# Kernel optimization log

Hardware: AMD Instinct MI355X
Metric: run time of the kernel (lower is better)

Reference implementation:

```python
import jax, jax.numpy as jnp
import numpy as np

B, S, H = 2, 4096, 1024
NH, BS, NR = 16, 64, 3
HD = H // NH
NB = S // BS
PEN = -10000.0


def setup_inputs():
    key = jax.random.key(0)
    k0, k1, k2, k3 = jax.random.split(key, 4)
    s = 0.02
    inp = {
        'hidden_states': jax.random.normal(k0, (B, S, H), jnp.float32),
        'attention_mask': jnp.ones((B, S), jnp.float32),
        'Wq': jax.random.normal(k1, (H, H), jnp.float32) * s,
        'Wk': jax.random.normal(k2, (H, H), jnp.float32) * s,
        'Wv': jax.random.normal(k3, (H, H), jnp.float32) * s,
        'bq': jnp.zeros((H,), jnp.float32),
        'bk': jnp.zeros((H,), jnp.float32),
        'bv': jnp.zeros((H,), jnp.float32),
    }
    rng = np.random.default_rng(0)
    inp['rand_attn'] = jnp.asarray(rng.integers(1, NB - 1, size=(B, NH, NB - 2, NR)), jnp.int32)
    return inp


def _attend(q_blk, kmat, vmat, mask, rsd):
    # q_blk:[b,h,q,d]  kmat/vmat:[b,h,k,d]  mask: multiplicative {0,1} broadcastable to [b,h,q,k]
    p = jnp.einsum('bhqd,bhkd->bhqk', q_blk, kmat) * rsd + (1.0 - mask) * PEN
    return jnp.einsum('bhqk,bhkd->bhqd', jax.nn.softmax(p, axis=-1), vmat)


def reference(hidden_states, attention_mask, Wq, bq, Wk, bk, Wv, bv, rand_attn):
    b, s, _ = hidden_states.shape
    h, d, bs = NH, HD, BS
    nb = s // bs
    rsd = 1.0 / jnp.sqrt(jnp.asarray(d, hidden_states.dtype))

    def proj(W, bias):
        return (hidden_states @ W + bias).reshape(b, s, h, d).transpose(0, 2, 1, 3)

    q, k, v = proj(Wq, bq), proj(Wk, bk), proj(Wv, bv)  # [b,h,s,d]

    # --- masks (create_masks_for_block_sparse_attn)
    bm = attention_mask.reshape(b, nb, bs)
    band_mask = jnp.einsum('blq,blk->blqk', bm[:, 2:-2],
                           jnp.concatenate([bm[:, 1:-3], bm[:, 2:-2], bm[:, 3:-1]], axis=2))[:, None]
    from_mask = attention_mask.reshape(b, 1, s, 1)
    to_mask = attention_mask.reshape(b, 1, 1, s)

    qb = q.reshape(b, h, nb, bs, d)
    kb = k.reshape(b, h, nb, bs, d)
    vb = v.reshape(b, h, nb, bs, d)

    # --- gather random blocks (jax_gather with batch_dims=2)
    gather2 = jax.vmap(jax.vmap(lambda m, i: m[i]))
    gk = gather2(kb, rand_attn).reshape(b, h, nb - 2, NR * bs, d)
    gv = gather2(vb, rand_attn).reshape(b, h, nb - 2, NR * bs, d)
    rm = jax.vmap(lambda m, i: m[i])(bm, rand_attn).reshape(b, h, nb - 2, NR * bs)
    rand_mask = jnp.einsum('blq,bhlk->bhlqk', bm[:, 1:-1], rm)  # [b,h,nb-2,bs,NR*bs]

    # --- block 0: attends to everything
    first_ctx = _attend(qb[:, :, 0], k, v, to_mask, rsd)[:, :, None]

    # --- block 1: first 3 blocks + last block + its random blocks
    ones_r = jnp.ones((b, 1, 1, NR * bs), q.dtype)
    sk = jnp.concatenate([kb[:, :, 0], kb[:, :, 1], kb[:, :, 2], kb[:, :, -1], gk[:, :, 0]], axis=2)
    sv = jnp.concatenate([vb[:, :, 0], vb[:, :, 1], vb[:, :, 2], vb[:, :, -1], gv[:, :, 0]], axis=2)
    seq_pad = jnp.concatenate([to_mask[:, :, :, :3 * bs], to_mask[:, :, :, -bs:], ones_r], axis=3)
    rand_pad = jnp.concatenate([jnp.ones((b, h, bs, 4 * bs), q.dtype), rand_mask[:, :, 0]], axis=3)
    second_ctx = _attend(qb[:, :, 1], sk, sv, jnp.minimum(seq_pad, rand_pad), rsd)[:, :, None]

    # --- middle blocks 2..nb-3: sliding band + random + first-global + last-global
    mq = qb[:, :, 2:-2]  # [b,h,L,bs,d], L = nb-4
    ek = jnp.concatenate([kb[:, :, 1:-3], kb[:, :, 2:-2], kb[:, :, 3:-1]], axis=3)  # [b,h,L,3bs,d]
    ev = jnp.concatenate([vb[:, :, 1:-3], vb[:, :, 2:-2], vb[:, :, 3:-1]], axis=3)
    band_p = jnp.einsum('bhlqd,bhlkd->bhlqk', mq, ek) * rsd + (1.0 - band_mask) * PEN
    rand_p = jnp.einsum('bhlqd,bhlkd->bhlqk', mq, gk[:, :, 1:-1]) * rsd + (1.0 - rand_mask[:, :, 1:-1]) * PEN
    first_p = jnp.einsum('bhlqd,bhkd->bhlqk', mq, kb[:, :, 0]) * rsd \
        + (1.0 - to_mask[:, :, :, :bs][:, :, :, None]) * PEN
    last_p = jnp.einsum('bhlqd,bhkd->bhlqk', mq, kb[:, :, -1]) * rsd \
        + (1.0 - to_mask[:, :, :, -bs:][:, :, :, None]) * PEN
    # scores layout: [first(bs) | band(3bs) | rand(NR*bs) | last(bs)]
    w = jax.nn.softmax(jnp.concatenate([first_p, band_p, rand_p, last_p], axis=-1), axis=-1)
    mid_ctx = jnp.einsum('bhlqk,bhlkd->bhlqd', w[..., bs:4 * bs], ev)
    mid_ctx += jnp.einsum('bhlqk,bhlkd->bhlqd', w[..., 4 * bs:-bs], gv[:, :, 1:-1])
    mid_ctx += jnp.einsum('bhlqk,bhkd->bhlqd', w[..., :bs], vb[:, :, 0])
    mid_ctx += jnp.einsum('bhlqk,bhkd->bhlqd', w[..., -bs:], vb[:, :, -1])

    # --- block nb-2: first block + last 3 blocks + its random blocks
    slk = jnp.concatenate([kb[:, :, 0], kb[:, :, -3], kb[:, :, -2], kb[:, :, -1], gk[:, :, -1]], axis=2)
    slv = jnp.concatenate([vb[:, :, 0], vb[:, :, -3], vb[:, :, -2], vb[:, :, -1], gv[:, :, -1]], axis=2)
    seq_pad = jnp.concatenate([to_mask[:, :, :, :bs], to_mask[:, :, :, -3 * bs:], ones_r], axis=3)
    rand_pad = jnp.concatenate([jnp.ones((b, h, bs, 4 * bs), q.dtype), rand_mask[:, :, -1]], axis=3)
    seclast_ctx = _attend(qb[:, :, -2], slk, slv, jnp.minimum(seq_pad, rand_pad), rsd)[:, :, None]

    # --- last block: attends to everything
    last_ctx = _attend(qb[:, :, -1], k, v, to_mask, rsd)[:, :, None]

    ctx = jnp.concatenate([first_ctx, second_ctx, mid_ctx, seclast_ctx, last_ctx], axis=2)
    ctx = ctx.reshape(b, h, s, d) * from_mask
    return ctx.transpose(0, 2, 1, 3).reshape(b, s, h * d)
```

## Files before the change

kernel.cpp:

```cpp
#include <hip/hip_runtime.h>

typedef unsigned short u16;
typedef short short8 __attribute__((ext_vector_type(8)));
typedef float f32x4 __attribute__((ext_vector_type(4)));

#define S_TOT 4096
#define NHEAD 16
#define HD 64
#define NB 64
#define BS 64
#define M0 16.0f

__device__ __forceinline__ u16 f2bf(float f) {
    unsigned int u = __builtin_bit_cast(unsigned int, f);
    unsigned int r = (u + 0x7fffu + ((u >> 16) & 1u)) >> 16;
    return (u16)r;
}

__device__ __forceinline__ void gload_lds16(const void* g, void* l) {
    __builtin_amdgcn_global_load_lds(
        (const __attribute__((address_space(1))) unsigned int*)g,
        (__attribute__((address_space(3))) unsigned int*)l, 16, 0, 0);
}

__device__ __forceinline__ float rsum16(float v) {
    v += __shfl_xor(v, 1);
    v += __shfl_xor(v, 2);
    v += __shfl_xor(v, 4);
    v += __shfl_xor(v, 8);
    return v;
}

__global__ __launch_bounds__(256) void convH(const float* __restrict__ h, u16* __restrict__ A) {
    size_t i = (size_t)blockIdx.x * blockDim.x + threadIdx.x;
    float4 v = ((const float4*)h)[i];
    ushort4 o;
    o.x = f2bf(v.x); o.y = f2bf(v.y); o.z = f2bf(v.z); o.w = f2bf(v.w);
    ((ushort4*)A)[i] = o;
}

__global__ __launch_bounds__(256) void transW(const float* __restrict__ Wq,
                                              const float* __restrict__ Wk,
                                              const float* __restrict__ Wv,
                                              u16* __restrict__ Wt) {
    const float* W = blockIdx.z == 0 ? Wq : (blockIdx.z == 1 ? Wk : Wv);
    u16* T = Wt + (size_t)blockIdx.z * 1024 * 1024;
    __shared__ float tile[64][65];
    int n0 = blockIdx.x * 64, k0 = blockIdx.y * 64;
    int tx = threadIdx.x, ty = threadIdx.y;
    for (int r = ty; r < 64; r += 4) tile[r][tx] = W[(size_t)(k0 + r) * 1024 + n0 + tx];
    __syncthreads();
    for (int r = ty; r < 64; r += 4) T[(size_t)(n0 + r) * 1024 + k0 + tx] = f2bf(tile[tx][r]);
}

__global__ __launch_bounds__(256, 2) void gemm_fused(const u16* __restrict__ Ah, const u16* __restrict__ Wt,
                                                     const float* __restrict__ bq, const float* __restrict__ bk,
                                                     const float* __restrict__ bv,
                                                     u16* __restrict__ Qb, u16* __restrict__ Kb,
                                                     u16* __restrict__ Vtb) {
    __shared__ alignas(16) char lds[2][32768];

    int bid = blockIdx.x;
    int xcd = bid & 7, idx = bid >> 3;
    int bm = xcd * 8 + (idx & 7);
    int bn = idx >> 3;
    int m0 = bm * 128, n0 = bn * 128;
    int mode = bn >> 3;
    const float* bias = mode == 0 ? bq : (mode == 1 ? bk : bv);
    int tid = threadIdx.x, wave = tid >> 6, lane = tid & 63;
    int lo = lane & 15, hi = lane >> 4;
    int wr = wave >> 1, wc = wave & 1;

    const char* Ac = (const char*)Ah;
    const char* Wc = (const char*)Wt;

    auto STAGE = [&](int buf, int t) {
#pragma unroll
        for (int i = 0; i < 4; i++) {
            int off = i * 4096 + tid * 16;
            int row = off >> 7, cb = off & 127;
            int cs = cb ^ ((row & 7) << 4);
            char* d = lds[buf] + i * 4096 + wave * 1024;
            gload_lds16(Ac + (size_t)(m0 + row) * 2048 + t * 128 + cs, d);
            gload_lds16(Wc + (size_t)(n0 + row) * 2048 + t * 128 + cs, d + 16384);
        }
    };

    f32x4 acc[4][4];
#pragma unroll
    for (int i = 0; i < 4; i++)
#pragma unroll
        for (int j = 0; j < 4; j++) acc[i][j] = f32x4{0.f, 0.f, 0.f, 0.f};

    STAGE(0, 0);
    asm volatile("s_waitcnt vmcnt(0)" ::: "memory");
    __builtin_amdgcn_s_barrier();
    __builtin_amdgcn_sched_barrier(0);

    for (int t = 0; t < 16; t++) {
        int buf = t & 1;
        if (t < 15) STAGE(buf ^ 1, t + 1);
        const char* As = lds[buf];
        const char* Bs = lds[buf] + 16384;
        short8 b[4][2];
#pragma unroll
        for (int ni = 0; ni < 4; ni++) {
            int row = wc * 64 + ni * 16 + lo;
            int sw = (row & 7) << 4;
#pragma unroll
            for (int kk = 0; kk < 2; kk++)
                b[ni][kk] = *(const short8*)(Bs + row * 128 + ((kk * 64 + hi * 16) ^ sw));
        }
        __builtin_amdgcn_s_setprio(1);
#pragma unroll
        for (int mi = 0; mi < 4; mi++) {
            int row = wr * 64 + mi * 16 + lo;
            int sw = (row & 7) << 4;
            short8 a0 = *(const short8*)(As + row * 128 + ((hi * 16) ^ sw));
            short8 a1 = *(const short8*)(As + row * 128 + ((64 + hi * 16) ^ sw));
#pragma unroll
            for (int ni = 0; ni < 4; ni++) {
                acc[mi][ni] = __builtin_amdgcn_mfma_f32_16x16x32_bf16(a0, b[ni][0], acc[mi][ni], 0, 0, 0);
                acc[mi][ni] = __builtin_amdgcn_mfma_f32_16x16x32_bf16(a1, b[ni][1], acc[mi][ni], 0, 0, 0);
            }
        }
        __builtin_amdgcn_s_setprio(0);
        asm volatile("s_waitcnt vmcnt(0)" ::: "memory");
        __builtin_amdgcn_s_barrier();
        __builtin_amdgcn_sched_barrier(0);
    }

    char* Cs = lds[0];
    int nb0 = n0 & 1023;
    float bv4[4];
#pragma unroll
    for (int ni = 0; ni < 4; ni++) bv4[ni] = bias[nb0 + wc * 64 + ni * 16 + lo];

    if (mode < 2) {
#pragma unroll
        for (int mi = 0; mi < 4; mi++)
#pragma unroll
            for (int ni = 0; ni < 4; ni++)
#pragma unroll
                for (int r = 0; r < 4; r++) {
                    int row = wr * 64 + mi * 16 + hi * 4 + r;
                    int nl = wc * 64 + ni * 16 + lo;
                    *(u16*)(Cs + ((row * 256 + nl * 2) ^ ((row & 7) << 4))) = f2bf(acc[mi][ni][r] + bv4[ni]);
                }
        __syncthreads();
        u16* T = (mode == 0) ? Qb : Kb;
#pragma unroll
        for (int it = 0; it < 8; it++) {
            int off = it * 4096 + tid * 16;
            int row = off >> 8, c = off & 255;
            short8 v = *(const short8*)(Cs + ((row * 256 + c) ^ ((row & 7) << 4)));
            int nm = nb0 + (c >> 1);
            int hh = nm >> 6, d = nm & 63;
            int s = m0 + row;
            int b_ = s >> 12, sr = s & 4095;
            *(short8*)&T[(((size_t)b_ * NHEAD + hh) * S_TOT + sr) * HD + d] = v;
        }
    } else {
#pragma unroll
        for (int mi = 0; mi < 4; mi++)
#pragma unroll
            for (int ni = 0; ni < 4; ni++)
#pragma unroll
                for (int r = 0; r < 4; r++) {
                    int row = wc * 64 + ni * 16 + lo;
                    int ml = wr * 64 + mi * 16 + hi * 4 + r;
                    *(u16*)(Cs + ((row * 256 + ml * 2) ^ ((row & 7) << 4))) = f2bf(acc[mi][ni][r] + bv4[ni]);
                }
        __syncthreads();
#pragma unroll
        for (int it = 0; it < 8; it++) {
            int off = it * 4096 + tid * 16;
            int row = off >> 8, c = off & 255;
            short8 v = *(const short8*)(Cs + ((row * 256 + c) ^ ((row & 7) << 4)));
            int dr = nb0 + row;
            int hh = dr >> 6, d = dr & 63;
            int s = m0 + (c >> 1);
            int b_ = s >> 12, sr = s & 4095;
            *(short8*)&Vtb[(((size_t)b_ * NHEAD + hh) * HD + d) * S_TOT + sr] = v;
        }
    }
}

__global__ __launch_bounds__(256) void bigbird_mid(const u16* __restrict__ Qb, const u16* __restrict__ Kb,
                                                   const u16* __restrict__ Vtb, const float* __restrict__ am,
                                                   const int* __restrict__ rand_attn, float* __restrict__ out) {
    int pid = blockIdx.x;
    int xcd = pid & 7, slot = pid >> 3;
    int bh = xcd * 4 + slot / 62;
    int l = slot % 62 + 1;
    int b = bh >> 4, h = bh & 15;
    const u16* Qh = Qb + (size_t)bh * S_TOT * HD;
    const u16* Kh = Kb + (size_t)bh * S_TOT * HD;
    const u16* Vh = Vtb + (size_t)bh * HD * S_TOT;
    int tid = threadIdx.x, wave = tid >> 6, lane = tid & 63;
    int lo = lane & 15, hi = lane >> 4;
    int kn = (l == 1 || l == 62) ? 7 : 8;

    __shared__ int klist[8];
    __shared__ float pen_lds[8][64];
    __shared__ alignas(16) u16 Kls[3][64 * 64];
    __shared__ alignas(16) u16 Vls[2][64 * 64];
    __shared__ alignas(16) u16 Plds[4][16 * 64];

    auto SK = [&](int s_, int kblk) {
        const char* Kc = (const char*)(Kh + (size_t)kblk * BS * HD);
#pragma unroll
        for (int i = 0; i < 2; i++) {
            int off = i * 4096 + wave * 1024 + lane * 16;
            int row = off >> 7, c = off & 127;
            gload_lds16(Kc + row * 128 + (c ^ ((row & 7) << 4)), (char*)Kls[s_] + i * 4096 + wave * 1024);
        }
    };
    auto SV = [&](int s_, int kblk) {
        const char* Vc = (const char*)(Vh + kblk * BS);
#pragma unroll
        for (int i = 0; i < 2; i++) {
            int off = i * 4096 + wave * 1024 + lane * 16;
            int row = off >> 7, c = off & 127;
            gload_lds16(Vc + (size_t)row * 8192 + (c ^ ((row & 7) << 4)), (char*)Vls[s_] + i * 4096 + wave * 1024);
        }
    };

    SK(0, 0);
    SV(0, 0);
    if (tid == 0) {
        int q = 0;
        klist[q++] = 0;
        if (l == 1) { klist[q++] = 1; klist[q++] = 2; }
        else if (l == 62) { klist[q++] = 61; klist[q++] = 62; }
        else { klist[q++] = l - 1; klist[q++] = l; klist[q++] = l + 1; }
        klist[q++] = 63;
        const int* ra = rand_attn + (((size_t)b * NHEAD + h) * 62 + (l - 1)) * 3;
        klist[q++] = ra[0]; klist[q++] = ra[1]; klist[q++] = ra[2];
    }
    __syncthreads();

#pragma unroll
    for (int it = 0; it < 2; it++) {
        int idx = it * 256 + tid;
        int ci = idx >> 6, col = idx & 63;
        if (ci < kn)
            pen_lds[ci][col] = (1.0f - am[b * S_TOT + klist[ci] * BS + col]) * (-10000.0f) - M0;
    }
    SK(1, klist[1]);
    __syncthreads();

    int qrow = l * BS + wave * 16;
    short8 qf[2];
#pragma unroll
    for (int kk = 0; kk < 2; kk++)
        qf[kk] = *(const short8*)&Qh[(size_t)(qrow + lo) * HD + kk * 32 + hi * 8];

    float ls[4];
    f32x4 oacc[4];
#pragma unroll
    for (int r = 0; r < 4; r++) ls[r] = 0.f;
#pragma unroll
    for (int n = 0; n < 4; n++) oacc[n] = f32x4{0.f, 0.f, 0.f, 0.f};
    char* pbase = (char*)&Plds[wave][0];

    for (int ci = 0; ci < kn; ci++) {
        if (ci + 1 < kn) SV((ci + 1) & 1, klist[ci + 1]);
        if (ci + 2 < kn) SK((ci + 2) % 3, klist[ci + 2]);
        const char* Kc = (const char*)Kls[ci % 3];
        const char* Vc = (const char*)Vls[ci & 1];
        float pen[4];
#pragma unroll
        for (int t = 0; t < 4; t++) pen[t] = pen_lds[ci][t * 16 + lo];
        f32x4 sc[4];
#pragma unroll
        for (int t = 0; t < 4; t++) {
            f32x4 c = f32x4{0.f, 0.f, 0.f, 0.f};
#pragma unroll
            for (int kk = 0; kk < 2; kk++) {
                int kr = t * 16 + lo;
                int a = (kr * 128 + kk * 64 + hi * 16) ^ ((kr & 7) << 4);
                short8 kf = *(const short8*)(Kc + a);
                c = __builtin_amdgcn_mfma_f32_16x16x32_bf16(qf[kk], kf, c, 0, 0, 0);
            }
            sc[t] = c;
        }
#pragma unroll
        for (int t = 0; t < 4; t++)
#pragma unroll
            for (int r = 0; r < 4; r++) {
                float pr = __expf(sc[t][r] * 0.125f + pen[t]);
                ls[r] += pr;
                int row = hi * 4 + r, col = t * 16 + lo;
                int off = (row * 128 + col * 2) ^ ((row & 7) << 4);
                *(u16*)(pbase + off) = f2bf(pr);
            }
#pragma unroll
        for (int kk = 0; kk < 2; kk++) {
            int off = (lo * 128 + kk * 64 + hi * 16) ^ ((lo & 7) << 4);
            short8 pf = *(const short8*)(pbase + off);
#pragma unroll
            for (int n = 0; n < 4; n++) {
                int vr = n * 16 + lo;
                int a = (vr * 128 + kk * 64 + hi * 16) ^ ((vr & 7) << 4);
                short8 vf = *(const short8*)(Vc + a);
                oacc[n] = __builtin_amdgcn_mfma_f32_16x16x32_bf16(pf, vf, oacc[n], 0, 0, 0);
            }
        }
        if (ci + 1 < kn) {
            if (ci + 2 < kn) {
                asm volatile("s_waitcnt vmcnt(2)" ::: "memory");
            } else {
                asm volatile("s_waitcnt vmcnt(0)" ::: "memory");
            }
            __builtin_amdgcn_s_barrier();
            __builtin_amdgcn_sched_barrier(0);
        }
    }

#pragma unroll
    for (int r = 0; r < 4; r++) {
        float lsum = rsum16(ls[r]);
        int q = qrow + hi * 4 + r;
        float qm = am[b * S_TOT + q];
        float iv = qm / lsum;
#pragma unroll
        for (int n = 0; n < 4; n++)
            out[((size_t)b * S_TOT + q) * 1024 + h * HD + n * 16 + lo] = oacc[n][r] * iv;
    }
}

__global__ __launch_bounds__(256) void bigbird_heavy(const u16* __restrict__ Qb, const u16* __restrict__ Kb,
                                                     const u16* __restrict__ Vtb, const float* __restrict__ am,
                                                     float* __restrict__ po, float* __restrict__ pl) {
    int pid = blockIdx.x;
    int xcd = pid & 7, slot = pid >> 3;
    int bh = xcd * 4 + (slot >> 5);
    int rem = slot & 31;
    int hv = rem >> 4, p = rem & 15;
    int l = hv ? 63 : 0;
    int b = bh >> 4;
    const u16* Qh = Qb + (size_t)bh * S_TOT * HD;
    const u16* Kh = Kb + (size_t)bh * S_TOT * HD;
    const u16* Vh = Vtb + (size_t)bh * HD * S_TOT;
    int tid = threadIdx.x, wave = tid >> 6, lane = tid & 63;
    int lo = lane & 15, hi = lane >> 4;

    __shared__ float pen_lds[4][64];
    __shared__ alignas(16) u16 Kls[3][64 * 64];
    __shared__ alignas(16) u16 Vls[2][64 * 64];
    __shared__ alignas(16) u16 Plds[4][16 * 64];

    auto SK = [&](int s_, int kblk) {
        const char* Kc = (const char*)(Kh + (size_t)kblk * BS * HD);
#pragma unroll
        for (int i = 0; i < 2; i++) {
            int off = i * 4096 + wave * 1024 + lane * 16;
            int row = off >> 7, c = off & 127;
            gload_lds16(Kc + row * 128 + (c ^ ((row & 7) << 4)), (char*)Kls[s_] + i * 4096 + wave * 1024);
        }
    };
    auto SV = [&](int s_, int kblk) {
        const char* Vc = (const char*)(Vh + kblk * BS);
#pragma unroll
        for (int i = 0; i < 2; i++) {
            int off = i * 4096 + wave * 1024 + lane * 16;
            int row = off >> 7, c = off & 127;
            gload_lds16(Vc + (size_t)row * 8192 + (c ^ ((row & 7) << 4)), (char*)Vls[s_] + i * 4096 + wave * 1024);
        }
    };

    int c0 = p * 4;
    SK(0, c0);
    SV(0, c0);
    {
        int ci = tid >> 6, col = tid & 63;
        pen_lds[ci][col] = (1.0f - am[b * S_TOT + (c0 + ci) * BS + col]) * (-10000.0f) - M0;
    }
    SK(1, c0 + 1);
    __syncthreads();

    int qrow = l * BS + wave * 16;
    short8 qf[2];
#pragma unroll
    for (int kk = 0; kk < 2; kk++)
        qf[kk] = *(const short8*)&Qh[(size_t)(qrow + lo) * HD + kk * 32 + hi * 8];

    float ls[4];
    f32x4 oacc[4];
#pragma unroll
    for (int r = 0; r < 4; r++) ls[r] = 0.f;
#pragma unroll
    for (int n = 0; n < 4; n++) oacc[n] = f32x4{0.f, 0.f, 0.f, 0.f};
    char* pbase = (char*)&Plds[wave][0];

#pragma unroll
    for (int ci = 0; ci < 4; ci++) {
        if (ci + 1 < 4) SV((ci + 1) & 1, c0 + ci + 1);
        if (ci + 2 < 4) SK((ci + 2) % 3, c0 + ci + 2);
        const char* Kc = (const char*)Kls[ci % 3];
        const char* Vc = (const char*)Vls[ci & 1];
        float pen[4];
#pragma unroll
        for (int t = 0; t < 4; t++) pen[t] = pen_lds[ci][t * 16 + lo];
        f32x4 sc[4];
#pragma unroll
        for (int t = 0; t < 4; t++) {
            f32x4 c = f32x4{0.f, 0.f, 0.f, 0.f};
#pragma unroll
            for (int kk = 0; kk < 2; kk++) {
                int kr = t * 16 + lo;
                int a = (kr * 128 + kk * 64 + hi * 16) ^ ((kr & 7) << 4);
                short8 kf = *(const short8*)(Kc + a);
                c = __builtin_amdgcn_mfma_f32_16x16x32_bf16(qf[kk], kf, c, 0, 0, 0);
            }
            sc[t] = c;
        }
#pragma unroll
        for (int t = 0; t < 4; t++)
#pragma unroll
            for (int r = 0; r < 4; r++) {
                float pr = __expf(sc[t][r] * 0.125f + pen[t]);
                ls[r] += pr;
                int row = hi * 4 + r, col = t * 16 + lo;
                int off = (row * 128 + col * 2) ^ ((row & 7) << 4);
                *(u16*)(pbase + off) = f2bf(pr);
            }
#pragma unroll
        for (int kk = 0; kk < 2; kk++) {
            int off = (lo * 128 + kk * 64 + hi * 16) ^ ((lo & 7) << 4);
            short8 pf = *(const short8*)(pbase + off);
#pragma unroll
            for (int n = 0; n < 4; n++) {
                int vr = n * 16 + lo;
                int a = (vr * 128 + kk * 64 + hi * 16) ^ ((vr & 7) << 4);
                short8 vf = *(const short8*)(Vc + a);
                oacc[n] = __builtin_amdgcn_mfma_f32_16x16x32_bf16(pf, vf, oacc[n], 0, 0, 0);
            }
        }
        if (ci + 1 < 4) {
            if (ci + 2 < 4) {
                asm volatile("s_waitcnt vmcnt(2)" ::: "memory");
            } else {
                asm volatile("s_waitcnt vmcnt(0)" ::: "memory");
            }
            __builtin_amdgcn_s_barrier();
            __builtin_amdgcn_sched_barrier(0);
        }
    }

    int combo = (bh << 1) | hv;
    int base = (combo * 16 + p) * 64;
#pragma unroll
    for (int r = 0; r < 4; r++) {
        int qr = wave * 16 + hi * 4 + r;
        float lsum = rsum16(ls[r]);
        if (lo == 0) pl[base + qr] = lsum;
#pragma unroll
        for (int n = 0; n < 4; n++)
            po[(size_t)(base + qr) * 64 + n * 16 + lo] = oacc[n][r];
    }
}

__global__ __launch_bounds__(256) void reduce_heavy(const float* __restrict__ po, const float* __restrict__ pl,
                                                    const float* __restrict__ am, float* __restrict__ out) {
    int combo = blockIdx.x;
    int b = combo >> 5, h = (combo >> 1) & 15, hv = combo & 1;
    int l = hv ? 63 : 0;
    for (int idx = threadIdx.x; idx < 4096; idx += 256) {
        int qr = idx >> 6, d = idx & 63;
        float s = 0.f, lsum = 0.f;
#pragma unroll
        for (int p = 0; p < 16; p++) {
            s += po[(size_t)((combo * 16 + p) * 64 + qr) * 64 + d];
            lsum += pl[(combo * 16 + p) * 64 + qr];
        }
        int q = l * BS + qr;
        float qm = am[b * S_TOT + q];
        out[((size_t)b * S_TOT + q) * 1024 + h * HD + d] = s / lsum * qm;
    }
}

extern "C" void kernel_launch(void* const* d_in, const int* in_sizes, int n_in,
                              void* d_out, int out_size, void* d_ws, size_t ws_size,
                              hipStream_t stream) {
    const float* hidden = (const float*)d_in[0];
    const float* am = (const float*)d_in[1];
    const float* Wq = (const float*)d_in[2];
    const float* Wk = (const float*)d_in[3];
    const float* Wv = (const float*)d_in[4];
    const float* bq = (const float*)d_in[5];
    const float* bk = (const float*)d_in[6];
    const float* bv = (const float*)d_in[7];
    const int* rand_attn = (const int*)d_in[8];
    float* out = (float*)d_out;

    char* w = (char*)d_ws;
    u16* Ah = (u16*)w;  w += (size_t)8192 * 1024 * 2;
    u16* Wt = (u16*)w;  w += (size_t)3 * 1024 * 1024 * 2;
    u16* Qb = (u16*)w;  w += (size_t)2 * 16 * 4096 * 64 * 2;
    u16* Kb = (u16*)w;  w += (size_t)2 * 16 * 4096 * 64 * 2;
    u16* Vtb = (u16*)w;
    float* po = (float*)Ah;
    float* pl = (float*)Wt;

    convH<<<8192, 256, 0, stream>>>(hidden, Ah);
    transW<<<dim3(16, 16, 3), dim3(64, 4), 0, stream>>>(Wq, Wk, Wv, Wt);
    gemm_fused<<<1536, 256, 0, stream>>>(Ah, Wt, bq, bk, bv, Qb, Kb, Vtb);
    bigbird_mid<<<1984, 256, 0, stream>>>(Qb, Kb, Vtb, am, rand_attn, out);
    bigbird_heavy<<<1024, 256, 0, stream>>>(Qb, Kb, Vtb, am, po, pl);
    reduce_heavy<<<64, 256, 0, stream>>>(po, pl, am, out);
}
```

Baseline: 146.5 us.

## Share K/V block loads across four query blocks per workgroup in BigBird attention

```diff
diff --git a/kernel.cpp b/kernel.cpp
--- a/kernel.cpp
+++ b/kernel.cpp
@@ -191,21 +191,21 @@
                                                    const int* __restrict__ rand_attn, float* __restrict__ out) {
     int pid = blockIdx.x;
     int xcd = pid & 7, slot = pid >> 3;
-    int bh = xcd * 4 + slot / 62;
-    int l = slot % 62 + 1;
+    int bh = xcd * 4 + (slot >> 4);
+    int grp = slot & 15;
+    int la = grp * 4 + 1;
     int b = bh >> 4, h = bh & 15;
     const u16* Qh = Qb + (size_t)bh * S_TOT * HD;
     const u16* Kh = Kb + (size_t)bh * S_TOT * HD;
     const u16* Vh = Vtb + (size_t)bh * HD * S_TOT;
     int tid = threadIdx.x, wave = tid >> 6, lane = tid & 63;
     int lo = lane & 15, hi = lane >> 4;
-    int kn = (l == 1 || l == 62) ? 7 : 8;
-
-    __shared__ int klist[8];
-    __shared__ float pen_lds[8][64];
+
+    __shared__ int klist[20];
+    __shared__ float pen_lds[20][64];
     __shared__ alignas(16) u16 Kls[3][64 * 64];
     __shared__ alignas(16) u16 Vls[2][64 * 64];
-    __shared__ alignas(16) u16 Plds[4][16 * 64];
+    __shared__ alignas(16) u16 Plds[4][64 * 64];
 
     auto SK = [&](int s_, int kblk) {
         const char* Kc = (const char*)(Kh + (size_t)kblk * BS * HD);
@@ -229,86 +229,128 @@
     SK(0, 0);
     SV(0, 0);
     if (tid == 0) {
-        int q = 0;
-        klist[q++] = 0;
-        if (l == 1) { klist[q++] = 1; klist[q++] = 2; }
-        else if (l == 62) { klist[q++] = 61; klist[q++] = 62; }
-        else { klist[q++] = l - 1; klist[q++] = l; klist[q++] = l + 1; }
-        klist[q++] = 63;
-        const int* ra = rand_attn + (((size_t)b * NHEAD + h) * 62 + (l - 1)) * 3;
-        klist[q++] = ra[0]; klist[q++] = ra[1]; klist[q++] = ra[2];
+        klist[0] = 0;
+        for (int s = 1; s <= 6; s++) {
+            int wblk = la - 1 + (s - 1);
+            klist[s] = wblk > 63 ? 63 : wblk;
+        }
+        klist[7] = 63;
+        for (int w = 0; w < 4; w++) {
+            int lw = la + w;
+            if (lw <= 62) {
+                const int* ra = rand_attn + ((size_t)bh * 62 + (lw - 1)) * 3;
+                klist[8 + 3 * w] = ra[0]; klist[9 + 3 * w] = ra[1]; klist[10 + 3 * w] = ra[2];
+            } else {
+                klist[8 + 3 * w] = 1; klist[9 + 3 * w] = 1; klist[10 + 3 * w] = 1;
+            }
+        }
     }
     __syncthreads();
 
 #pragma unroll
-    for (int it = 0; it < 2; it++) {
+    for (int it = 0; it < 5; it++) {
         int idx = it * 256 + tid;
         int ci = idx >> 6, col = idx & 63;
-        if (ci < kn)
+        if (ci < 20)
             pen_lds[ci][col] = (1.0f - am[b * S_TOT + klist[ci] * BS + col]) * (-10000.0f) - M0;
     }
     SK(1, klist[1]);
     __syncthreads();
 
-    int qrow = l * BS + wave * 16;
-    short8 qf[2];
-#pragma unroll
-    for (int kk = 0; kk < 2; kk++)
-        qf[kk] = *(const short8*)&Qh[(size_t)(qrow + lo) * HD + kk * 32 + hi * 8];
-
-    float ls[4];
-    f32x4 oacc[4];
-#pragma unroll
-    for (int r = 0; r < 4; r++) ls[r] = 0.f;
-#pragma unroll
-    for (int n = 0; n < 4; n++) oacc[n] = f32x4{0.f, 0.f, 0.f, 0.f};
+    int l = la + wave;
+    bool act = (l <= 62);
+    unsigned mask = 0;
+    if (act) {
+        mask = (1u << 0) | (1u << 7) | (7u << (8 + 3 * wave));
+        for (int s = 1; s <= 6; s++) {
+            int wblk = la - 1 + (s - 1);
+            int d = wblk - l;
+            if (d >= -1 && d <= 1 && wblk >= 1 && wblk <= 62) mask |= 1u << s;
+        }
+    }
+
+    short8 qf[4][2];
+    if (act) {
+#pragma unroll
+        for (int mi = 0; mi < 4; mi++)
+#pragma unroll
+            for (int kk = 0; kk < 2; kk++)
+                qf[mi][kk] = *(const short8*)&Qh[(size_t)(l * BS + mi * 16 + lo) * HD + kk * 32 + hi * 8];
+    }
+
+    float ls[4][4];
+    f32x4 oacc[4][4];
+#pragma unroll
+    for (int mi = 0; mi < 4; mi++)
+#pragma unroll
+        for (int r = 0; r < 4; r++) ls[mi][r] = 0.f;
+#pragma unroll
+    for (int mi = 0; mi < 4; mi++)
+#pragma unroll
+        for (int n = 0; n < 4; n++) oacc[mi][n] = f32x4{0.f, 0.f, 0.f, 0.f};
     char* pbase = (char*)&Plds[wave][0];
 
-    for (int ci = 0; ci < kn; ci++) {
-        if (ci + 1 < kn) SV((ci + 1) & 1, klist[ci + 1]);
-        if (ci + 2 < kn) SK((ci + 2) % 3, klist[ci + 2]);
-        const char* Kc = (const char*)Kls[ci % 3];
-        const char* Vc = (const char*)Vls[ci & 1];
-        float pen[4];
-#pragma unroll
-        for (int t = 0; t < 4; t++) pen[t] = pen_lds[ci][t * 16 + lo];
-        f32x4 sc[4];
-#pragma unroll
-        for (int t = 0; t < 4; t++) {
-            f32x4 c = f32x4{0.f, 0.f, 0.f, 0.f};
-#pragma unroll
-            for (int kk = 0; kk < 2; kk++) {
-                int kr = t * 16 + lo;
-                int a = (kr * 128 + kk * 64 + hi * 16) ^ ((kr & 7) << 4);
-                short8 kf = *(const short8*)(Kc + a);
-                c = __builtin_amdgcn_mfma_f32_16x16x32_bf16(qf[kk], kf, c, 0, 0, 0);
-            }
-            sc[t] = c;
-        }
-#pragma unroll
-        for (int t = 0; t < 4; t++)
-#pragma unroll
-            for (int r = 0; r < 4; r++) {
-                float pr = __expf(sc[t][r] * 0.125f + pen[t]);
-                ls[r] += pr;
-                int row = hi * 4 + r, col = t * 16 + lo;
-                int off = (row * 128 + col * 2) ^ ((row & 7) << 4);
-                *(u16*)(pbase + off) = f2bf(pr);
-            }
-#pragma unroll
-        for (int kk = 0; kk < 2; kk++) {
-            int off = (lo * 128 + kk * 64 + hi * 16) ^ ((lo & 7) << 4);
-            short8 pf = *(const short8*)(pbase + off);
-#pragma unroll
-            for (int n = 0; n < 4; n++) {
-                int vr = n * 16 + lo;
-                int a = (vr * 128 + kk * 64 + hi * 16) ^ ((vr & 7) << 4);
-                short8 vf = *(const short8*)(Vc + a);
-                oacc[n] = __builtin_amdgcn_mfma_f32_16x16x32_bf16(pf, vf, oacc[n], 0, 0, 0);
-            }
-        }
-        if (ci + 1 < kn) {
-            if (ci + 2 < kn) {
+    for (int ci = 0; ci < 20; ci++) {
+        if (ci + 1 < 20) SV((ci + 1) & 1, klist[ci + 1]);
+        if (ci + 2 < 20) SK((ci + 2) % 3, klist[ci + 2]);
+        if ((mask >> ci) & 1) {
+            const char* Kc = (const char*)Kls[ci % 3];
+            const char* Vc = (const char*)Vls[ci & 1];
+            short8 kf[8];
+#pragma unroll
+            for (int t = 0; t < 4; t++)
+#pragma unroll
+                for (int kk = 0; kk < 2; kk++) {
+                    int kr = t * 16 + lo;
+                    kf[t * 2 + kk] = *(const short8*)(Kc + ((kr * 128 + kk * 64 + hi * 16) ^ ((kr & 7) << 4)));
+                }
+            float pen[4];
+#pragma unroll
+            for (int t = 0; t < 4; t++) pen[t] = pen_lds[ci][t * 16 + lo];
+#pragma unroll
+            for (int mi = 0; mi < 4; mi++) {
+                f32x4 sc[4];
+#pragma unroll
+                for (int t = 0; t < 4; t++) {
+                    f32x4 c = f32x4{0.f, 0.f, 0.f, 0.f};
+#pragma unroll
+                    for (int kk = 0; kk < 2; kk++)
+                        c = __builtin_amdgcn_mfma_f32_16x16x32_bf16(qf[mi][kk], kf[t * 2 + kk], c, 0, 0, 0);
+                    sc[t] = c;
+                }
+#pragma unroll
+                for (int t = 0; t < 4; t++)
+#pragma unroll
+                    for (int r = 0; r < 4; r++) {
+                        float pr = __expf(sc[t][r] * 0.125f + pen[t]);
+                        ls[mi][r] += pr;
+                        int row = mi * 16 + hi * 4 + r, col = t * 16 + lo;
+                        int off = (row * 128 + col * 2) ^ ((row & 7) << 4);
+                        *(u16*)(pbase + off) = f2bf(pr);
+                    }
+            }
+            short8 vf[8];
+#pragma unroll
+            for (int n = 0; n < 4; n++)
+#pragma unroll
+                for (int kk = 0; kk < 2; kk++) {
+                    int vr = n * 16 + lo;
+                    vf[n * 2 + kk] = *(const short8*)(Vc + ((vr * 128 + kk * 64 + hi * 16) ^ ((vr & 7) << 4)));
+                }
+#pragma unroll
+            for (int mi = 0; mi < 4; mi++)
+#pragma unroll
+                for (int kk = 0; kk < 2; kk++) {
+                    int prow = mi * 16 + lo;
+                    int off = (prow * 128 + kk * 64 + hi * 16) ^ ((prow & 7) << 4);
+                    short8 pf = *(const short8*)(pbase + off);
+#pragma unroll
+                    for (int n = 0; n < 4; n++)
+                        oacc[mi][n] = __builtin_amdgcn_mfma_f32_16x16x32_bf16(pf, vf[n * 2 + kk], oacc[mi][n], 0, 0, 0);
+                }
+        }
+        if (ci + 1 < 20) {
+            if (ci + 2 < 20) {
                 asm volatile("s_waitcnt vmcnt(2)" ::: "memory");
             } else {
                 asm volatile("s_waitcnt vmcnt(0)" ::: "memory");
@@ -318,15 +360,19 @@
         }
     }
 
-#pragma unroll
-    for (int r = 0; r < 4; r++) {
-        float lsum = rsum16(ls[r]);
-        int q = qrow + hi * 4 + r;
-        float qm = am[b * S_TOT + q];
-        float iv = qm / lsum;
-#pragma unroll
-        for (int n = 0; n < 4; n++)
-            out[((size_t)b * S_TOT + q) * 1024 + h * HD + n * 16 + lo] = oacc[n][r] * iv;
+    if (act) {
+#pragma unroll
+        for (int mi = 0; mi < 4; mi++)
+#pragma unroll
+            for (int r = 0; r < 4; r++) {
+                float lsum = rsum16(ls[mi][r]);
+                int q = l * BS + mi * 16 + hi * 4 + r;
+                float qm = am[b * S_TOT + q];
+                float iv = qm / lsum;
+#pragma unroll
+                for (int n = 0; n < 4; n++)
+                    out[((size_t)b * S_TOT + q) * 1024 + h * HD + n * 16 + lo] = oacc[mi][n][r] * iv;
+            }
     }
 }
 
@@ -335,21 +381,22 @@
                                                      float* __restrict__ po, float* __restrict__ pl) {
     int pid = blockIdx.x;
     int xcd = pid & 7, slot = pid >> 3;
-    int bh = xcd * 4 + (slot >> 5);
-    int rem = slot & 31;
-    int hv = rem >> 4, p = rem & 15;
-    int l = hv ? 63 : 0;
+    int bh = xcd * 4 + (slot >> 3);
+    int p = slot & 7;
     int b = bh >> 4;
     const u16* Qh = Qb + (size_t)bh * S_TOT * HD;
     const u16* Kh = Kb + (size_t)bh * S_TOT * HD;
     const u16* Vh = Vtb + (size_t)bh * HD * S_TOT;
     int tid = threadIdx.x, wave = tid >> 6, lane = tid & 63;
     int lo = lane & 15, hi = lane >> 4;
-
-    __shared__ float pen_lds[4][64];
+    int hv = wave >> 1;
+    int l = hv ? 63 : 0;
+    int rowoff = (wave & 1) * 32;
+
+    __shared__ float pen_lds[8][64];
     __shared__ alignas(16) u16 Kls[3][64 * 64];
     __shared__ alignas(16) u16 Vls[2][64 * 64];
-    __shared__ alignas(16) u16 Plds[4][16 * 64];
+    __shared__ alignas(16) u16 Plds[4][32 * 64];
 
     auto SK = [&](int s_, int kblk) {
         const char* Kc = (const char*)(Kh + (size_t)kblk * BS * HD);
@@ -370,76 +417,96 @@
         }
     };
 
-    int c0 = p * 4;
+    int c0 = p * 8;
     SK(0, c0);
     SV(0, c0);
-    {
-        int ci = tid >> 6, col = tid & 63;
+#pragma unroll
+    for (int it = 0; it < 2; it++) {
+        int idx = it * 256 + tid;
+        int ci = idx >> 6, col = idx & 63;
         pen_lds[ci][col] = (1.0f - am[b * S_TOT + (c0 + ci) * BS + col]) * (-10000.0f) - M0;
     }
     SK(1, c0 + 1);
     __syncthreads();
 
-    int qrow = l * BS + wave * 16;
-    short8 qf[2];
-#pragma unroll
-    for (int kk = 0; kk < 2; kk++)
-        qf[kk] = *(const short8*)&Qh[(size_t)(qrow + lo) * HD + kk * 32 + hi * 8];
-
-    float ls[4];
-    f32x4 oacc[4];
-#pragma unroll
-    for (int r = 0; r < 4; r++) ls[r] = 0.f;
-#pragma unroll
-    for (int n = 0; n < 4; n++) oacc[n] = f32x4{0.f, 0.f, 0.f, 0.f};
+    short8 qf[2][2];
+#pragma unroll
+    for (int mi = 0; mi < 2; mi++)
+#pragma unroll
+        for (int kk = 0; kk < 2; kk++)
+            qf[mi][kk] = *(const short8*)&Qh[(size_t)(l * BS + rowoff + mi * 16 + lo) * HD + kk * 32 + hi * 8];
+
+    float ls[2][4];
+    f32x4 oacc[2][4];
+#pragma unroll
+    for (int mi = 0; mi < 2; mi++)
+#pragma unroll
+        for (int r = 0; r < 4; r++) ls[mi][r] = 0.f;
+#pragma unroll
+    for (int mi = 0; mi < 2; mi++)
+#pragma unroll
+        for (int n = 0; n < 4; n++) oacc[mi][n] = f32x4{0.f, 0.f, 0.f, 0.f};
     char* pbase = (char*)&Plds[wave][0];
 
-#pragma unroll
-    for (int ci = 0; ci < 4; ci++) {
-        if (ci + 1 < 4) SV((ci + 1) & 1, c0 + ci + 1);
-        if (ci + 2 < 4) SK((ci + 2) % 3, c0 + ci + 2);
+    for (int ci = 0; ci < 8; ci++) {
+        if (ci + 1 < 8) SV((ci + 1) & 1, c0 + ci + 1);
+        if (ci + 2 < 8) SK((ci + 2) % 3, c0 + ci + 2);
         const char* Kc = (const char*)Kls[ci % 3];
         const char* Vc = (const char*)Vls[ci & 1];
-        float pen[4];
-#pragma unroll
-        for (int t = 0; t < 4; t++) pen[t] = pen_lds[ci][t * 16 + lo];
-        f32x4 sc[4];
-#pragma unroll
-        for (int t = 0; t < 4; t++) {
-            f32x4 c = f32x4{0.f, 0.f, 0.f, 0.f};
+        short8 kf[8];
+#pragma unroll
+        for (int t = 0; t < 4; t++)
 #pragma unroll
             for (int kk = 0; kk < 2; kk++) {
                 int kr = t * 16 + lo;
-                int a = (kr * 128 + kk * 64 + hi * 16) ^ ((kr & 7) << 4);
-                short8 kf = *(const short8*)(Kc + a);
-                c = __builtin_amdgcn_mfma_f32_16x16x32_bf16(qf[kk], kf, c, 0, 0, 0);
-            }
-            sc[t] = c;
-        }
-#pragma unroll
-        for (int t = 0; t < 4; t++)
-#pragma unroll
-            for (int r = 0; r < 4; r++) {
-                float pr = __expf(sc[t][r] * 0.125f + pen[t]);
-                ls[r] += pr;
-                int row = hi * 4 + r, col = t * 16 + lo;
-                int off = (row * 128 + col * 2) ^ ((row & 7) << 4);
-                *(u16*)(pbase + off) = f2bf(pr);
-            }
-#pragma unroll
-        for (int kk = 0; kk < 2; kk++) {
-            int off = (lo * 128 + kk * 64 + hi * 16) ^ ((lo & 7) << 4);
-            short8 pf = *(const short8*)(pbase + off);
-#pragma unroll
-            for (int n = 0; n < 4; n++) {
+                kf[t * 2 + kk] = *(const short8*)(Kc + ((kr * 128 + kk * 64 + hi * 16) ^ ((kr & 7) << 4)));
+            }
+        float pen[4];
+#pragma unroll
+        for (int t = 0; t < 4; t++) pen[t] = pen_lds[ci][t * 16 + lo];
+#pragma unroll
+        for (int mi = 0; mi < 2; mi++) {
+            f32x4 sc[4];
+#pragma unroll
+            for (int t = 0; t < 4; t++) {
+                f32x4 c = f32x4{0.f, 0.f, 0.f, 0.f};
+#pragma unroll
+                for (int kk = 0; kk < 2; kk++)
+                    c = __builtin_amdgcn_mfma_f32_16x16x32_bf16(qf[mi][kk], kf[t * 2 + kk], c, 0, 0, 0);
+                sc[t] = c;
+            }
+#pragma unroll
+            for (int t = 0; t < 4; t++)
+#pragma unroll
+                for (int r = 0; r < 4; r++) {
+                    float pr = __expf(sc[t][r] * 0.125f + pen[t]);
+                    ls[mi][r] += pr;
+                    int row = mi * 16 + hi * 4 + r, col = t * 16 + lo;
+                    int off = (row * 128 + col * 2) ^ ((row & 7) << 4);
+                    *(u16*)(pbase + off) = f2bf(pr);
+                }
+        }
+        short8 vf[8];
+#pragma unroll
+        for (int n = 0; n < 4; n++)
+#pragma unroll
+            for (int kk = 0; kk < 2; kk++) {
                 int vr = n * 16 + lo;
-                int a = (vr * 128 + kk * 64 + hi * 16) ^ ((vr & 7) << 4);
-                short8 vf = *(const short8*)(Vc + a);
-                oacc[n] = __builtin_amdgcn_mfma_f32_16x16x32_bf16(pf, vf, oacc[n], 0, 0, 0);
-            }
-        }
-        if (ci + 1 < 4) {
-            if (ci + 2 < 4) {
+                vf[n * 2 + kk] = *(const short8*)(Vc + ((vr * 128 + kk * 64 + hi * 16) ^ ((vr & 7) << 4)));
+            }
+#pragma unroll
+        for (int mi = 0; mi < 2; mi++)
+#pragma unroll
+            for (int kk = 0; kk < 2; kk++) {
+                int prow = mi * 16 + lo;
+                int off = (prow * 128 + kk * 64 + hi * 16) ^ ((prow & 7) << 4);
+                short8 pf = *(const short8*)(pbase + off);
+#pragma unroll
+                for (int n = 0; n < 4; n++)
+                    oacc[mi][n] = __builtin_amdgcn_mfma_f32_16x16x32_bf16(pf, vf[n * 2 + kk], oacc[mi][n], 0, 0, 0);
+            }
+        if (ci + 1 < 8) {
+            if (ci + 2 < 8) {
                 asm volatile("s_waitcnt vmcnt(2)" ::: "memory");
             } else {
                 asm volatile("s_waitcnt vmcnt(0)" ::: "memory");
@@ -450,16 +517,18 @@
     }
 
     int combo = (bh << 1) | hv;
-    int base = (combo * 16 + p) * 64;
-#pragma unroll
-    for (int r = 0; r < 4; r++) {
-        int qr = wave * 16 + hi * 4 + r;
-        float lsum = rsum16(ls[r]);
-        if (lo == 0) pl[base + qr] = lsum;
-#pragma unroll
-        for (int n = 0; n < 4; n++)
-            po[(size_t)(base + qr) * 64 + n * 16 + lo] = oacc[n][r];
-    }
+    int base = (combo * 8 + p) * 64;
+#pragma unroll
+    for (int mi = 0; mi < 2; mi++)
+#pragma unroll
+        for (int r = 0; r < 4; r++) {
+            int qr = rowoff + mi * 16 + hi * 4 + r;
+            float lsum = rsum16(ls[mi][r]);
+            if (lo == 0) pl[base + qr] = lsum;
+#pragma unroll
+            for (int n = 0; n < 4; n++)
+                po[(size_t)(base + qr) * 64 + n * 16 + lo] = oacc[mi][n][r];
+        }
 }
 
 __global__ __launch_bounds__(256) void reduce_heavy(const float* __restrict__ po, const float* __restrict__ pl,
@@ -471,9 +540,9 @@
         int qr = idx >> 6, d = idx & 63;
         float s = 0.f, lsum = 0.f;
 #pragma unroll
-        for (int p = 0; p < 16; p++) {
-            s += po[(size_t)((combo * 16 + p) * 64 + qr) * 64 + d];
-            lsum += pl[(combo * 16 + p) * 64 + qr];
+        for (int p = 0; p < 8; p++) {
+            s += po[(size_t)((combo * 8 + p) * 64 + qr) * 64 + d];
+            lsum += pl[(combo * 8 + p) * 64 + qr];
         }
         int q = l * BS + qr;
         float qm = am[b * S_TOT + q];
@@ -507,7 +576,7 @@
     convH<<<8192, 256, 0, stream>>>(hidden, Ah);
     transW<<<dim3(16, 16, 3), dim3(64, 4), 0, stream>>>(Wq, Wk, Wv, Wt);
     gemm_fused<<<1536, 256, 0, stream>>>(Ah, Wt, bq, bk, bv, Qb, Kb, Vtb);
-    bigbird_mid<<<1984, 256, 0, stream>>>(Qb, Kb, Vtb, am, rand_attn, out);
-    bigbird_heavy<<<1024, 256, 0, stream>>>(Qb, Kb, Vtb, am, po, pl);
+    bigbird_mid<<<512, 256, 0, stream>>>(Qb, Kb, Vtb, am, rand_attn, out);
+    bigbird_heavy<<<256, 256, 0, stream>>>(Qb, Kb, Vtb, am, po, pl);
     reduce_heavy<<<64, 256, 0, stream>>>(po, pl, am, out);
 }
```

Result: slower. 199.7 us (+36.4%).
